# Kernel optimization log

Hardware: AMD Instinct MI355X
Metric: run time of the kernel (lower is better)

Reference implementation:

```python
import jax, jax.numpy as jnp
import numpy as np

NEG_SLOPE = 0.2

def gat_conv(x, src, dst, W, a_src, a_dst, b, num_nodes, concat):
    # PyG GATConv (add_self_loops already applied to src/dst).
    H, C = a_src.shape
    h = (x @ W).reshape(-1, H, C)                      # [N,H,C]
    s = jnp.einsum('nhc,hc->nh', h, a_src)             # per-node src score
    d = jnp.einsum('nhc,hc->nh', h, a_dst)             # per-node dst score
    e = jax.nn.leaky_relu(s[src] + d[dst], NEG_SLOPE)  # [E,H]
    emax = jax.lax.stop_gradient(
        jax.ops.segment_max(e, dst, num_segments=num_nodes))  # [N,H]
    ex = jnp.exp(e - emax[dst])
    denom = jax.ops.segment_sum(ex, dst, num_segments=num_nodes)
    alpha = ex / denom[dst]                            # segment softmax over in-edges
    msg = h[src] * alpha[:, :, None]                   # [E,H,C]
    out = jax.ops.segment_sum(msg, dst, num_segments=num_nodes)
    out = out.reshape(num_nodes, H * C) if concat else out.mean(axis=1)
    return out + b

def setup_inputs() -> dict:
    key = jax.random.key(0)
    ks = jax.random.split(key, 20)
    N, E, F = 50000, 400000, 256
    x = jax.random.normal(ks[0], (N, F), dtype=jnp.float32)
    edge_index = jax.random.randint(ks[1], (2, E), 0, N, dtype=jnp.int64)
    def p(k, shape):
        return (jax.random.normal(k, shape, dtype=jnp.float32) * 0.1)
    inp = {'x': x, 'edge_index': edge_index}
    # conv1: 256 -> 8x32 ; conv2: 256 -> 4x32 ; conv3: 128 -> 2x32 ; conv4: 64 -> 1x32
    dims = [(256, 8, 32), (256, 4, 32), (128, 2, 32), (64, 1, 32)]
    ki = 2
    for i, (fin, H, C) in enumerate(dims, start=1):
        inp[f'W{i}'] = p(ks[ki], (fin, H * C)); ki += 1
        inp[f'a_src{i}'] = p(ks[ki], (H, C)); ki += 1
        inp[f'a_dst{i}'] = p(ks[ki], (H, C)); ki += 1
        bdim = H * C if i < 4 else C
        inp[f'b{i}'] = jnp.zeros((bdim,), dtype=jnp.float32)
    return inp

def reference(x, edge_index, W1, a_src1, a_dst1, b1, W2, a_src2, a_dst2, b2,
              W3, a_src3, a_dst3, b3, W4, a_src4, a_dst4, b4):
    N = x.shape[0]
    loops = jnp.arange(N, dtype=edge_index.dtype)
    src = jnp.concatenate([edge_index[0], loops])
    dst = jnp.concatenate([edge_index[1], loops])
    h = jax.nn.elu(gat_conv(x, src, dst, W1, a_src1, a_dst1, b1, N, True))
    h = jax.nn.elu(gat_conv(h, src, dst, W2, a_src2, a_dst2, b2, N, True))
    h = gat_conv(h, src, dst, W3, a_src3, a_dst3, b3, N, True)
    h = jax.nn.elu(h)
    h = gat_conv(h, src, dst, W4, a_src4, a_dst4, b4, N, False)
    return jax.nn.log_softmax(h, axis=1)
```

## Files before the change

### kernel.cpp

```cpp
#include <hip/hip_runtime.h>
#include <hip/hip_bf16.h>

#define LRELU_SLOPE 0.2f

typedef __attribute__((ext_vector_type(8))) short short8;
typedef __attribute__((ext_vector_type(4))) float f32x4;

__device__ __forceinline__ unsigned short bf16r(float f) {
    unsigned int u = __builtin_bit_cast(unsigned int, f);
    u += 0x7fffu + ((u >> 16) & 1u);
    return (unsigned short)(u >> 16);
}
__device__ __forceinline__ float bf2f(unsigned short u) {
    return __builtin_bit_cast(float, (unsigned int)u << 16);
}


#define WTOT 108544

__global__ void k_pre(const float* __restrict__ Wa, const float* __restrict__ Wb,
                      const float* __restrict__ Wc, const float* __restrict__ Wd,
                      unsigned short* __restrict__ Ta, unsigned short* __restrict__ Tb,
                      unsigned short* __restrict__ Tc, unsigned short* __restrict__ Td,
                      const int* __restrict__ ei, int* __restrict__ cnt, int E, int N) {
    int gid = blockIdx.x * blockDim.x + threadIdx.x;
    if (gid < WTOT) {
        int id = gid;
        const float* W; unsigned short* T; int K, Nc;
        if (id < 65536)       { W = Wa; T = Ta; K = 256; Nc = 256; }
        else if (id < 98304)  { id -= 65536;  W = Wb; T = Tb; K = 256; Nc = 128; }
        else if (id < 106496) { id -= 98304;  W = Wc; T = Tc; K = 128; Nc = 64; }
        else                  { id -= 106496; W = Wd; T = Td; K = 64;  Nc = 32; }
        int n = id / K, k = id % K;
        T[id] = bf16r(W[(long)k * Nc + n]);
        return;
    }
    int e = gid - WTOT;
    if (e >= E + N) return;
    int dst = (e < E) ? ei[E + e] : (e - E);
    atomicAdd(&cnt[dst], 1);
}


__global__ void k_scan_blk(const int* __restrict__ cnt, int* __restrict__ offs,
                           int* __restrict__ bsum, int N) {
    __shared__ int temp[1024];
    int t = threadIdx.x;
    int gi = blockIdx.x * 1024 + t;
    int v = (gi < N) ? cnt[gi] : 0;
    temp[t] = v;
    __syncthreads();
    for (int o = 1; o < 1024; o <<= 1) {
        int x = (t >= o) ? temp[t - o] : 0;
        __syncthreads();
        temp[t] += x;
        __syncthreads();
    }
    if (gi < N) offs[gi] = temp[t] - v;
    if (t == 1023) bsum[blockIdx.x] = temp[1023];
}

__global__ void k_scan(const int* __restrict__ cnt, int* __restrict__ offs, int N) {
    __shared__ int temp[1024];
    __shared__ int carry_s;
    int t = threadIdx.x;
    if (t == 0) carry_s = 0;
    __syncthreads();
    for (int base = 0; base < N; base += 1024) {
        int v = (base + t < N) ? cnt[base + t] : 0;
        temp[t] = v;
        __syncthreads();
        for (int o = 1; o < 1024; o <<= 1) {
            int x = (t >= o) ? temp[t - o] : 0;
            __syncthreads();
            temp[t] += x;
            __syncthreads();
        }
        int incl = temp[t];
        int carry = carry_s;
        if (base + t < N) offs[base + t] = carry + incl - v;
        __syncthreads();
        if (t == 1023) carry_s = carry + temp[1023];
        __syncthreads();
    }
    if (t == 0) offs[N] = carry_s;
}

__global__ void k_scan_add(int* __restrict__ offs, const int* __restrict__ bpre,
                           int* __restrict__ wp, int N, int nb) {
    int gi = blockIdx.x * blockDim.x + threadIdx.x;
    if (gi < N) {
        int v = offs[gi] + bpre[gi >> 10];
        offs[gi] = v;
        wp[gi] = v;
    } else if (gi == N) {
        offs[N] = bpre[nb];
    }
}

__global__ void k_scatter(const int* __restrict__ ei, int* __restrict__ wp,
                          int* __restrict__ adj, int E, int N) {
    int e = blockIdx.x * blockDim.x + threadIdx.x;
    if (e >= E + N) return;
    int srcn = (e < E) ? ei[e] : (e - E);
    int dst  = (e < E) ? ei[E + e] : (e - E);
    int pos = atomicAdd(&wp[dst], 1);
    adj[pos] = srcn;
}


template<int BN, int KT, int GX, bool F32A>
__global__ __launch_bounds__(256, 4) void k_mgemm(const void* __restrict__ Ain,
                                               const unsigned short* __restrict__ WT,
                                               unsigned short* __restrict__ Cb,
                                               const float* __restrict__ a_src,
                                               const float* __restrict__ a_dst,
                                               float* __restrict__ sbuf,
                                               float* __restrict__ dbuf,
                                               int M, int Nc, int H, int RB) {
    constexpr int KITER = KT / 32;
    constexpr int KS  = KT + 8;
    constexpr int NBF = BN / 16;
    constexpr int CPR = BN / 32;
    constexpr int SP  = BN + 8;
    constexpr int STAGE = BN * KS;
    constexpr int EPIL  = 64 * SP;
    constexpr int LBSZ  = STAGE > EPIL ? STAGE : EPIL;
    __shared__ __align__(16) unsigned short LB[LBSZ];

    int id = blockIdx.x;
    int xcd = id & 7;
    int q  = id >> 3;
    int ct = q % GX;
    int rb = (q / GX) * 8 + xcd;
    if (rb >= RB) return;
    int bm = rb * 64, bn = ct * BN;

    int t = threadIdx.x;
    int wv = t >> 6, l = t & 63;
    int row_in = l & 15, quad = l >> 4;

    int grA = min(bm + wv * 16 + row_in, M - 1);
    const float* Af = (const float*)Ain;
    const unsigned short* Ab = (const unsigned short*)Ain;
    short8 areg[KITER];
    if constexpr (F32A) {
        float4 af0[KITER], af1[KITER];
#pragma unroll
        for (int ki = 0; ki < KITER; ++ki) {
            const float4* p = (const float4*)&Af[(long)grA * KT + ki * 32 + quad * 8];
            af0[ki] = p[0];
            af1[ki] = p[1];
        }
#pragma unroll
        for (int ki = 0; ki < KITER; ++ki) {
            float4 f0 = af0[ki], f1 = af1[ki];
            short8 av;
            av[0] = (short)bf16r(f0.x); av[1] = (short)bf16r(f0.y);
            av[2] = (short)bf16r(f0.z); av[3] = (short)bf16r(f0.w);
            av[4] = (short)bf16r(f1.x); av[5] = (short)bf16r(f1.y);
            av[6] = (short)bf16r(f1.z); av[7] = (short)bf16r(f1.w);
            areg[ki] = av;
        }
    } else {
#pragma unroll
        for (int ki = 0; ki < KITER; ++ki)
            areg[ki] = *(const short8*)&Ab[(long)grA * KT + ki * 32 + quad * 8];
    }

    constexpr int PER = BN * (KT / 8) / 256;
#pragma unroll
    for (int i = 0; i < PER; ++i) {
        int ch = t + i * 256;
        int col = ch / (KT / 8);
        int kc  = ch % (KT / 8);
        int gcol = min(bn + col, Nc - 1);
        *(short8*)&LB[col * KS + kc * 8] = *(const short8*)&WT[(long)gcol * KT + kc * 8];
    }
    __syncthreads();

    f32x4 acc[NBF];
#pragma unroll
    for (int j = 0; j < NBF; ++j) acc[j] = (f32x4){0.f, 0.f, 0.f, 0.f};

#pragma unroll
    for (int ki = 0; ki < KITER; ++ki) {
        short8 av = areg[ki];
#pragma unroll
        for (int f = 0; f < NBF; ++f) {
            short8 bv = *(const short8*)&LB[(f * 16 + row_in) * KS + ki * 32 + quad * 8];
            acc[f] = __builtin_amdgcn_mfma_f32_16x16x32_bf16(av, bv, acc[f], 0, 0, 0);
        }
    }
    __syncthreads();

#pragma unroll
    for (int r = 0; r < 4; ++r)
#pragma unroll
        for (int f = 0; f < NBF; ++f)
            LB[(wv * 16 + quad * 4 + r) * SP + f * 16 + row_in] = bf16r(acc[f][r]);
    __syncthreads();

    int rr = t / CPR, cc = t % CPR;
    if (rr < 64) {
        int grow = bm + rr;
        int colb = bn + cc * 32;
        if (grow < M && colb < Nc) {
            const unsigned short* ep = &LB[rr * SP + cc * 32];
            short8 v0 = *(const short8*)(ep);
            short8 v1 = *(const short8*)(ep + 8);
            short8 v2 = *(const short8*)(ep + 16);
            short8 v3 = *(const short8*)(ep + 24);
            unsigned short* cp = &Cb[(long)grow * Nc + colb];
            *(short8*)(cp)      = v0;
            *(short8*)(cp + 8)  = v1;
            *(short8*)(cp + 16) = v2;
            *(short8*)(cp + 24) = v3;
            int hd = colb >> 5;
            const float* ap = a_src + hd * 32;
            const float* dp = a_dst + hd * 32;
            float ss = 0.f, dd = 0.f;
#pragma unroll
            for (int u = 0; u < 8; ++u) {
                float va = bf2f((unsigned short)v0[u]); ss += va * ap[u];      dd += va * dp[u];
                float vb = bf2f((unsigned short)v1[u]); ss += vb * ap[8 + u];  dd += vb * dp[8 + u];
                float vc = bf2f((unsigned short)v2[u]); ss += vc * ap[16 + u]; dd += vc * dp[16 + u];
                float vd = bf2f((unsigned short)v3[u]); ss += vd * ap[24 + u]; dd += vd * dp[24 + u];
            }
            sbuf[(long)grow * H + hd] = ss;
            dbuf[(long)grow * H + hd] = dd;
        }
    }
}


#define QB(v, k) __builtin_amdgcn_ds_swizzle((v), 0x8000 | ((k) * 0x55))

template<int ACT>
__global__ void k_aggf(const unsigned short* __restrict__ h, const float* __restrict__ s,
                       const float* __restrict__ dsc, const int* __restrict__ offs,
                       const int* __restrict__ adj, const float* __restrict__ bias,
                       unsigned short* __restrict__ out16, float* __restrict__ out32,
                       int N, int H) {
    const int C8 = 4;
    long tid = (long)blockIdx.x * blockDim.x + threadIdx.x;
    int HC8 = H * C8;
    if (tid >= (long)N * HC8) return;
    int c8 = (int)(tid % C8);
    int hh = (int)((tid / C8) % H);
    int n  = (int)(tid / HC8);
    int beg = offs[n], end = offs[n + 1];
    float dn = dsc[n * H + hh];
    int HC = HC8 * 8;
    int coff = hh * 32 + c8 * 8;
    const unsigned short* hb = h + coff;

    float denom = 0.f;
    float acc[8];
#pragma unroll
    for (int u = 0; u < 8; ++u) acc[u] = 0.f;

    for (int j = beg; j < end; j += 4) {
        int my = j + c8;
        int idx = my < end ? my : end - 1;
        int sn = adj[idx];
        float e = s[sn * H + hh] + dn;
        e = e > 0.f ? e : LRELU_SLOPE * e;
        float w = __expf(fminf(e, 80.f));
        if (my >= end) w = 0.f;
        int wi = __builtin_bit_cast(int, w);
        int sn0 = QB(sn, 0);
        int sn1 = QB(sn, 1);
        int sn2 = QB(sn, 2);
        int sn3 = QB(sn, 3);
        float w0 = __builtin_bit_cast(float, QB(wi, 0));
        float w1 = __builtin_bit_cast(float, QB(wi, 1));
        float w2 = __builtin_bit_cast(float, QB(wi, 2));
        float w3 = __builtin_bit_cast(float, QB(wi, 3));
        short8 h0 = *(const short8*)(hb + (size_t)sn0 * HC);
        short8 h1 = *(const short8*)(hb + (size_t)sn1 * HC);
        short8 h2 = *(const short8*)(hb + (size_t)sn2 * HC);
        short8 h3 = *(const short8*)(hb + (size_t)sn3 * HC);
        denom += (w0 + w1) + (w2 + w3);
#pragma unroll
        for (int u = 0; u < 8; ++u) {
            float a01 = w0 * bf2f((unsigned short)h0[u]) + w1 * bf2f((unsigned short)h1[u]);
            float a23 = w2 * bf2f((unsigned short)h2[u]) + w3 * bf2f((unsigned short)h3[u]);
            acc[u] += a01 + a23;
        }
    }

    float inv = 1.0f / denom;
    float o[8];
#pragma unroll
    for (int u = 0; u < 8; ++u) o[u] = acc[u] * inv + bias[coff + u];

    if (ACT == 1) {
        short8 pk;
#pragma unroll
        for (int u = 0; u < 8; ++u) {
            float v = o[u] > 0.f ? o[u] : (__expf(o[u]) - 1.f);
            pk[u] = (short)bf16r(v);
        }
        *(short8*)(out16 + tid * 8) = pk;
    } else {
        float m = o[0];
#pragma unroll
        for (int u = 1; u < 8; ++u) m = fmaxf(m, o[u]);
        m = fmaxf(m, __shfl_xor(m, 1));
        m = fmaxf(m, __shfl_xor(m, 2));
        float ssum = 0.f;
#pragma unroll
        for (int u = 0; u < 8; ++u) ssum += __expf(o[u] - m);
        ssum += __shfl_xor(ssum, 1);
        ssum += __shfl_xor(ssum, 2);
        float lse = m + __logf(ssum);
        float4 lo = {o[0] - lse, o[1] - lse, o[2] - lse, o[3] - lse};
        float4 hi = {o[4] - lse, o[5] - lse, o[6] - lse, o[7] - lse};
        *(float4*)(out32 + tid * 8)     = lo;
        *(float4*)(out32 + tid * 8 + 4) = hi;
    }
}


static inline size_t align_up(size_t x) { return (x + 255) & ~(size_t)255; }

extern "C" void kernel_launch(void* const* d_in, const int* in_sizes, int n_in,
                              void* d_out, int out_size, void* d_ws, size_t ws_size,
                              hipStream_t stream) {
    const float* x   = (const float*)d_in[0];
    const int*   ei  = (const int*)d_in[1];

    const int N = in_sizes[0] / 256;
    const int E = in_sizes[1] / 2;
    const int ET = E + N;
    const int NB = (N + 1023) / 1024;

    size_t off = 0;
    char* ws = (char*)d_ws;
    auto take = [&](size_t bytes) { char* p = ws + off; off += align_up(bytes); return p; };
    int*   offs  = (int*)take((size_t)(N + 1) * 4);
    int*   wp    = (int*)take((size_t)N * 4);
    int*   adj   = (int*)take((size_t)ET * 4);
    int*   bsum  = (int*)take((size_t)(NB + 1) * 4);
    int*   bpre  = (int*)take((size_t)(NB + 1) * 4);
    float* sbuf  = (float*)take((size_t)N * 8 * 4);
    float* dbuf  = (float*)take((size_t)N * 8 * 4);
    unsigned short* Xb = (unsigned short*)take((size_t)N * 256 * 2);
    unsigned short* Yb = (unsigned short*)take((size_t)N * 256 * 2);
    unsigned short* WT0 = (unsigned short*)take((size_t)256 * 256 * 2);
    unsigned short* WT1 = (unsigned short*)take((size_t)256 * 128 * 2);
    unsigned short* WT2 = (unsigned short*)take((size_t)128 * 64 * 2);
    unsigned short* WT3 = (unsigned short*)take((size_t)64 * 32 * 2);
    (void)ws_size;

    hipMemsetAsync(wp, 0, (size_t)N * 4, stream);
    {
        long tot = WTOT + ET;
        k_pre<<<(int)((tot + 255) / 256), 256, 0, stream>>>(
            (const float*)d_in[2], (const float*)d_in[6], (const float*)d_in[10],
            (const float*)d_in[14], WT0, WT1, WT2, WT3, ei, wp, E, N);
        k_scan_blk<<<NB, 1024, 0, stream>>>(wp, offs, bsum, N);
        k_scan<<<1, 1024, 0, stream>>>(bsum, bpre, NB);
        k_scan_add<<<(N + 256) / 256, 256, 0, stream>>>(offs, bpre, wp, N, NB);
        k_scatter<<<(ET + 255) / 256, 256, 0, stream>>>(ei, wp, adj, E, N);
    }

    const float* as_[4] = {(const float*)d_in[3], (const float*)d_in[7],
                           (const float*)d_in[11], (const float*)d_in[15]};
    const float* ad_[4] = {(const float*)d_in[4], (const float*)d_in[8],
                           (const float*)d_in[12], (const float*)d_in[16]};
    const float* b_[4]  = {(const float*)d_in[5], (const float*)d_in[9],
                           (const float*)d_in[13], (const float*)d_in[17]};
    int H_[4] = {8, 4, 2, 1};

    const int RB  = (N + 63) / 64;
    const int RBp = ((RB + 7) / 8) * 8;

    for (int li = 0; li < 4; ++li) {
        int H = H_[li];

        if (li == 0) {
            k_mgemm<64, 256, 4, true><<<4 * RBp, 256, 0, stream>>>(
                x, WT0, Yb, as_[0], ad_[0], sbuf, dbuf, N, 256, H, RB);
        } else if (li == 1) {
            k_mgemm<64, 256, 2, false><<<2 * RBp, 256, 0, stream>>>(
                Xb, WT1, Yb, as_[1], ad_[1], sbuf, dbuf, N, 128, H, RB);
        } else if (li == 2) {
            k_mgemm<64, 128, 1, false><<<RBp, 256, 0, stream>>>(
                Xb, WT2, Yb, as_[2], ad_[2], sbuf, dbuf, N, 64, H, RB);
        } else {
            k_mgemm<32, 64, 1, false><<<RBp, 256, 0, stream>>>(
                Xb, WT3, Yb, as_[3], ad_[3], sbuf, dbuf, N, 32, H, RB);
        }
        {
            long total = (long)N * H * 4;
            int nb = (int)((total + 255) / 256);
            if (li < 3)
                k_aggf<1><<<nb, 256, 0, stream>>>(Yb, sbuf, dbuf, offs, adj, b_[li],
                                                  Xb, nullptr, N, H);
            else
                k_aggf<0><<<nb, 256, 0, stream>>>(Yb, sbuf, dbuf, offs, adj, b_[li],
                                                  nullptr, (float*)d_out, N, H);
        }
    }
}
```

Measured before the change: 317.8 us.

## Pre-convert x to bf16 and stage GEMM tiles via direct global-to-LDS loads

Converts the fp32 input x to bf16 once in the preprocessing kernel. Layer 1 therefore reads bf16, and its GEMM no longer reconverts the same rows for each of the four column tiles. The GEMM now loads both the A and B tiles with global_load_lds into an XOR-swizzled LDS layout instead of register and padded-LDS loads, and reads them back through swizzled offsets. The launch-bounds occupancy hint is dropped. In exchange there is an extra N×256 bf16 write and read, and LDS use per block grows, which may lower occupancy.

```diff
diff --git a/kernel.cpp b/kernel.cpp
--- a/kernel.cpp
+++ b/kernel.cpp
@@ -15,17 +15,35 @@
     return __builtin_bit_cast(float, (unsigned int)u << 16);
 }
 
+#define GLD16(g, l)                                                            \
+    __builtin_amdgcn_global_load_lds(                                          \
+        (const __attribute__((address_space(1))) void*)(g),                    \
+        (__attribute__((address_space(3))) void*)(l), 16, 0, 0)
+
 
 #define WTOT 108544
 
-__global__ void k_pre(const float* __restrict__ Wa, const float* __restrict__ Wb,
+__global__ void k_pre(const float* __restrict__ x, unsigned short* __restrict__ Xb,
+                      const float* __restrict__ Wa, const float* __restrict__ Wb,
                       const float* __restrict__ Wc, const float* __restrict__ Wd,
                       unsigned short* __restrict__ Ta, unsigned short* __restrict__ Tb,
                       unsigned short* __restrict__ Tc, unsigned short* __restrict__ Td,
-                      const int* __restrict__ ei, int* __restrict__ cnt, int E, int N) {
+                      const int* __restrict__ ei, int* __restrict__ cnt,
+                      int XC, int E, int N) {
     int gid = blockIdx.x * blockDim.x + threadIdx.x;
-    if (gid < WTOT) {
-        int id = gid;
+    if (gid < XC) {
+        const float4* xp = (const float4*)x + (long)gid * 2;
+        float4 a = xp[0], b = xp[1];
+        short8 pk;
+        pk[0] = (short)bf16r(a.x); pk[1] = (short)bf16r(a.y);
+        pk[2] = (short)bf16r(a.z); pk[3] = (short)bf16r(a.w);
+        pk[4] = (short)bf16r(b.x); pk[5] = (short)bf16r(b.y);
+        pk[6] = (short)bf16r(b.z); pk[7] = (short)bf16r(b.w);
+        *(short8*)(Xb + (long)gid * 8) = pk;
+        return;
+    }
+    int id = gid - XC;
+    if (id < WTOT) {
         const float* W; unsigned short* T; int K, Nc;
         if (id < 65536)       { W = Wa; T = Ta; K = 256; Nc = 256; }
         else if (id < 98304)  { id -= 65536;  W = Wb; T = Tb; K = 256; Nc = 128; }
@@ -35,7 +53,7 @@
         T[id] = bf16r(W[(long)k * Nc + n]);
         return;
     }
-    int e = gid - WTOT;
+    int e = id - WTOT;
     if (e >= E + N) return;
     int dst = (e < E) ? ei[E + e] : (e - E);
     atomicAdd(&cnt[dst], 1);
@@ -109,8 +127,8 @@
 }
 
 
-template<int BN, int KT, int GX, bool F32A>
-__global__ __launch_bounds__(256, 4) void k_mgemm(const void* __restrict__ Ain,
+template<int BN, int KT, int GX>
+__global__ __launch_bounds__(256) void k_mgemm(const unsigned short* __restrict__ Ab,
                                                const unsigned short* __restrict__ WT,
                                                unsigned short* __restrict__ Cb,
                                                const float* __restrict__ a_src,
@@ -119,13 +137,15 @@
                                                float* __restrict__ dbuf,
                                                int M, int Nc, int H, int RB) {
     constexpr int KITER = KT / 32;
-    constexpr int KS  = KT + 8;
     constexpr int NBF = BN / 16;
     constexpr int CPR = BN / 32;
     constexpr int SP  = BN + 8;
-    constexpr int STAGE = BN * KS;
-    constexpr int EPIL  = 64 * SP;
-    constexpr int LBSZ  = STAGE > EPIL ? STAGE : EPIL;
+    constexpr int ASH = 64 * KT;
+    constexpr int BSH = BN * KT;
+    constexpr int EPIL = 64 * SP;
+    constexpr int LBSZ = (ASH + BSH) > EPIL ? (ASH + BSH) : EPIL;
+    constexpr int SHC = (KT == 256) ? 5 : (KT == 128 ? 4 : 3);
+    constexpr int BIT = BN * KT / 2048;
     __shared__ __align__(16) unsigned short LB[LBSZ];
 
     int id = blockIdx.x;
@@ -139,56 +159,43 @@
     int t = threadIdx.x;
     int wv = t >> 6, l = t & 63;
     int row_in = l & 15, quad = l >> 4;
-
-    int grA = min(bm + wv * 16 + row_in, M - 1);
-    const float* Af = (const float*)Ain;
-    const unsigned short* Ab = (const unsigned short*)Ain;
-    short8 areg[KITER];
-    if constexpr (F32A) {
-        float4 af0[KITER], af1[KITER];
-#pragma unroll
-        for (int ki = 0; ki < KITER; ++ki) {
-            const float4* p = (const float4*)&Af[(long)grA * KT + ki * 32 + quad * 8];
-            af0[ki] = p[0];
-            af1[ki] = p[1];
-        }
-#pragma unroll
-        for (int ki = 0; ki < KITER; ++ki) {
-            float4 f0 = af0[ki], f1 = af1[ki];
-            short8 av;
-            av[0] = (short)bf16r(f0.x); av[1] = (short)bf16r(f0.y);
-            av[2] = (short)bf16r(f0.z); av[3] = (short)bf16r(f0.w);
-            av[4] = (short)bf16r(f1.x); av[5] = (short)bf16r(f1.y);
-            av[6] = (short)bf16r(f1.z); av[7] = (short)bf16r(f1.w);
-            areg[ki] = av;
-        }
-    } else {
-#pragma unroll
-        for (int ki = 0; ki < KITER; ++ki)
-            areg[ki] = *(const short8*)&Ab[(long)grA * KT + ki * 32 + quad * 8];
-    }
-
-    constexpr int PER = BN * (KT / 8) / 256;
-#pragma unroll
-    for (int i = 0; i < PER; ++i) {
-        int ch = t + i * 256;
-        int col = ch / (KT / 8);
-        int kc  = ch % (KT / 8);
-        int gcol = min(bn + col, Nc - 1);
-        *(short8*)&LB[col * KS + kc * 8] = *(const short8*)&WT[(long)gcol * KT + kc * 8];
-    }
+    char* LBb = (char*)LB;
+
+    long abyte = (long)bm * (KT * 2);
+    long mbyte = (long)M * (KT * 2);
+    const char* Agb = (const char*)Ab;
+#pragma unroll
+    for (int i = 0; i < KITER; ++i) {
+        int c = i * 256 + t;
+        int cs = c ^ ((c >> SHC) & 7);
+        long gb = abyte + (long)cs * 16;
+        if (gb >= mbyte) gb = abyte;
+        GLD16(Agb + gb, LBb + (i * 256 + wv * 64) * 16);
+    }
+    const char* WTb = (const char*)WT + (long)bn * (KT * 2);
+#pragma unroll
+    for (int i = 0; i < BIT; ++i) {
+        int c = i * 256 + t;
+        int cs = c ^ ((c >> SHC) & 7);
+        GLD16(WTb + (long)cs * 16, LBb + ASH * 2 + (i * 256 + wv * 64) * 16);
+    }
+    asm volatile("s_waitcnt vmcnt(0)" ::: "memory");
     __syncthreads();
 
     f32x4 acc[NBF];
 #pragma unroll
     for (int j = 0; j < NBF; ++j) acc[j] = (f32x4){0.f, 0.f, 0.f, 0.f};
 
+    int arow = wv * 16 + row_in;
 #pragma unroll
     for (int ki = 0; ki < KITER; ++ki) {
-        short8 av = areg[ki];
+        int aoff = (arow * (KT * 2) + ki * 64 + quad * 16) ^ ((arow & 7) << 4);
+        short8 av = *(const short8*)(LBb + aoff);
 #pragma unroll
         for (int f = 0; f < NBF; ++f) {
-            short8 bv = *(const short8*)&LB[(f * 16 + row_in) * KS + ki * 32 + quad * 8];
+            int bcol = f * 16 + row_in;
+            int boff = ASH * 2 + ((bcol * (KT * 2) + ki * 64 + quad * 16) ^ ((bcol & 7) << 4));
+            short8 bv = *(const short8*)(LBb + boff);
             acc[f] = __builtin_amdgcn_mfma_f32_16x16x32_bf16(av, bv, acc[f], 0, 0, 0);
         }
     }
@@ -335,6 +342,7 @@
     const int E = in_sizes[1] / 2;
     const int ET = E + N;
     const int NB = (N + 1023) / 1024;
+    const int XC = N * 32;
 
     size_t off = 0;
     char* ws = (char*)d_ws;
@@ -356,10 +364,11 @@
 
     hipMemsetAsync(wp, 0, (size_t)N * 4, stream);
     {
-        long tot = WTOT + ET;
+        long tot = (long)XC + WTOT + ET;
         k_pre<<<(int)((tot + 255) / 256), 256, 0, stream>>>(
+            x, Xb,
             (const float*)d_in[2], (const float*)d_in[6], (const float*)d_in[10],
-            (const float*)d_in[14], WT0, WT1, WT2, WT3, ei, wp, E, N);
+            (const float*)d_in[14], WT0, WT1, WT2, WT3, ei, wp, XC, E, N);
         k_scan_blk<<<NB, 1024, 0, stream>>>(wp, offs, bsum, N);
         k_scan<<<1, 1024, 0, stream>>>(bsum, bpre, NB);
         k_scan_add<<<(N + 256) / 256, 256, 0, stream>>>(offs, bpre, wp, N, NB);
@@ -381,16 +390,16 @@
         int H = H_[li];
 
         if (li == 0) {
-            k_mgemm<64, 256, 4, true><<<4 * RBp, 256, 0, stream>>>(
-                x, WT0, Yb, as_[0], ad_[0], sbuf, dbuf, N, 256, H, RB);
+            k_mgemm<64, 256, 4><<<4 * RBp, 256, 0, stream>>>(
+                Xb, WT0, Yb, as_[0], ad_[0], sbuf, dbuf, N, 256, H, RB);
         } else if (li == 1) {
-            k_mgemm<64, 256, 2, false><<<2 * RBp, 256, 0, stream>>>(
+            k_mgemm<64, 256, 2><<<2 * RBp, 256, 0, stream>>>(
                 Xb, WT1, Yb, as_[1], ad_[1], sbuf, dbuf, N, 128, H, RB);
         } else if (li == 2) {
-            k_mgemm<64, 128, 1, false><<<RBp, 256, 0, stream>>>(
+            k_mgemm<64, 128, 1><<<RBp, 256, 0, stream>>>(
                 Xb, WT2, Yb, as_[2], ad_[2], sbuf, dbuf, N, 64, H, RB);
         } else {
-            k_mgemm<32, 64, 1, false><<<RBp, 256, 0, stream>>>(
+            k_mgemm<32, 64, 1><<<RBp, 256, 0, stream>>>(
                 Xb, WT3, Yb, as_[3], ad_[3], sbuf, dbuf, N, 32, H, RB);
         }
         {
```

New measurement: 313.8 us. Within noise of the previous version (-1.2%).
